# Kernel tuning notes

Measured on AMD Instinct MI355X. Metric: run time of the kernel, lower is better.

The kernel has to match this reference:

```python
import jax, jax.numpy as jnp
import numpy as np

B, H, W, DIM, NH = 4, 32, 32, 768, 12
HD = DIM // NH

def setup_inputs() -> dict:
    key = jax.random.key(0)
    ks = jax.random.split(key, 7)
    s = 0.02
    return {
        "x": jax.random.normal(ks[0], (B, H, W, DIM), dtype=jnp.float32),
        "qkv_w": jax.random.normal(ks[1], (3 * DIM, DIM), dtype=jnp.float32) * s,  # torch Linear (out,in)
        "qkv_b": jax.random.normal(ks[2], (3 * DIM,), dtype=jnp.float32) * s,
        "proj_w": jax.random.normal(ks[3], (DIM, DIM), dtype=jnp.float32) * s,
        "proj_b": jax.random.normal(ks[4], (DIM,), dtype=jnp.float32) * s,
        "rel_pos_h": jax.random.normal(ks[5], (2 * H - 1, HD), dtype=jnp.float32) * s,
        "rel_pos_w": jax.random.normal(ks[6], (2 * W - 1, HD), dtype=jnp.float32) * s,
    }

def _get_rel_pos(size, rel_pos):
    # q_size == k_size == size, rel_pos.shape[0] == 2*size-1 -> no interpolation
    idx = jnp.arange(size)[:, None] - jnp.arange(size)[None, :] + (size - 1)
    return rel_pos[idx]  # (size, size, head_dim)

def reference(x, qkv_w, qkv_b, proj_w, proj_b, rel_pos_h, rel_pos_w):
    b, h, w, c = x.shape
    hw = h * w
    hd = c // NH
    scale = hd ** -0.5  # SDPA default scale

    qkv = x @ qkv_w.T + qkv_b                       # (B,H,W,3C)
    qkv = qkv.reshape(b, hw, 3, NH, hd).transpose(2, 0, 3, 1, 4)  # (3,B,nh,HW,hd)
    q, k, v = qkv[0], qkv[1], qkv[2]                # each (B,nh,HW,hd)

    Rh = _get_rel_pos(h, rel_pos_h)                 # (H,H,hd)
    Rw = _get_rel_pos(w, rel_pos_w)                 # (W,W,hd)
    r_q = q.reshape(b, NH, h, w, hd)
    rel_h = jnp.einsum('bnhwc,hkc->bnhwk', r_q, Rh)  # (B,nh,H,W,H)
    rel_w = jnp.einsum('bnhwc,wkc->bnhwk', r_q, Rw)  # (B,nh,H,W,W)
    bias = (rel_h[..., :, None] + rel_w[..., None, :]).reshape(b, NH, hw, hw)

    attn = jnp.einsum('bnqd,bnkd->bnqk', q, k) * scale + bias
    attn = jax.nn.softmax(attn, axis=-1)
    out = jnp.einsum('bnqk,bnkd->bnqd', attn, v)    # (B,nh,HW,hd)
    out = out.reshape(b, NH, h, w, hd).transpose(0, 2, 3, 1, 4).reshape(b, h, w, c)
    return out @ proj_w.T + proj_b
```

## Files before the change

### kernel.cpp

```cpp
#include <hip/hip_runtime.h>
#include <stdint.h>

typedef unsigned short u16;
typedef __attribute__((ext_vector_type(8))) short short8;
typedef __attribute__((ext_vector_type(8))) u16 ushort8;
typedef __attribute__((ext_vector_type(4))) float f32x4;
typedef __attribute__((ext_vector_type(16))) float f32x16;
typedef __attribute__((ext_vector_type(4))) unsigned int uint4v;

#define LOG2E 1.44269504088896f

__device__ __forceinline__ u16 f2bf(float f) {
  unsigned int u = __builtin_bit_cast(unsigned int, f);
  u += 0x7FFF + ((u >> 16) & 1);
  return (u16)(u >> 16);
}
__device__ __forceinline__ unsigned int cvtpk(float a, float b) {
  unsigned int r;
  asm("v_cvt_pk_bf16_f32 %0, %1, %2" : "=v"(r) : "v"(a), "v"(b));
  return r;
}
__device__ __forceinline__ void plswap(unsigned int& a, unsigned int& b) {
  asm("v_permlane32_swap_b32 %0, %1" : "+v"(a), "+v"(b));
}
__device__ __forceinline__ void gload_lds16(const u16* g, u16* l) {
  __builtin_amdgcn_global_load_lds((const __attribute__((address_space(1))) void*)g,
                                   (__attribute__((address_space(3))) void*)l, 16, 0, 0);
}

__global__ __launch_bounds__(256) void cvt_all(
    const float* __restrict__ s0, u16* __restrict__ d0, int n0,
    const float* __restrict__ s1, u16* __restrict__ d1, int n1,
    const float* __restrict__ s2, u16* __restrict__ d2, int n2,
    const float* __restrict__ s3, u16* __restrict__ d3, int n3,
    const float* __restrict__ s4, u16* __restrict__ d4, int n4) {
  const int tid0 = blockIdx.x * 256 + threadIdx.x;
  const int stride = gridDim.x * 256 * 4;
#define CVT_SEG(S, D, N)                                       \
  for (int i = tid0 * 4; i < (N); i += stride) {               \
    float4 v = *(const float4*)((S) + i);                      \
    *(uint2*)((D) + i) = make_uint2(cvtpk(v.x, v.y), cvtpk(v.z, v.w)); \
  }
  CVT_SEG(s0, d0, n0)
  CVT_SEG(s1, d1, n1)
  CVT_SEG(s2, d2, n2)
  CVT_SEG(s3, d3, n3)
  CVT_SEG(s4, d4, n4)
#undef CVT_SEG
}

#define CTS 130
__global__ __launch_bounds__(256) void gemm128q(
    const u16* __restrict__ A, const u16* __restrict__ B,
    const float* __restrict__ bias,
    u16* __restrict__ qo, u16* __restrict__ ko, u16* __restrict__ vto,
    int M, int N, int K) {
  __shared__ u16 smem[4 * 128 * 64];
  const int tid = threadIdx.x;
  const int lane = tid & 63, wave = tid >> 6;
  const int wr = wave >> 1, wc = wave & 1;
  const int l15 = lane & 15, l4 = lane >> 4;
  const int fid = blockIdx.y * gridDim.x + blockIdx.x;
  const int cpx = (gridDim.x * gridDim.y) >> 3;
  const int swz = (fid & 7) * cpx + (fid >> 3);
  const int bxs = swz % gridDim.x, bys = swz / gridDim.x;
  const int bm = bys << 7, bn = bxs << 7;
  f32x4 acc[4][4] = {};
  const int nkt = K >> 6;

#define STAGE(buf, kt)                                                        \
  {                                                                           \
    u16* As_ = smem + (buf) * 16384;                                          \
    u16* Bs_ = As_ + 8192;                                                    \
    const int k0_ = (kt) << 6;                                                \
    _Pragma("unroll") for (int j = 0; j < 4; ++j) {                           \
      const int cbase = j * 256 + wave * 64;                                  \
      const int chunk = cbase + lane;                                         \
      const int row = chunk >> 3;                                             \
      const int co = (((chunk & 7) ^ (row & 7)) << 3);                        \
      gload_lds16(A + (size_t)(bm + row) * K + k0_ + co, As_ + cbase * 8);    \
      gload_lds16(B + (size_t)(bn + row) * K + k0_ + co, Bs_ + cbase * 8);    \
    }                                                                         \
  }

  STAGE(0, 0)
  __syncthreads();
  int cur = 0;
  for (int kt = 0; kt < nkt; ++kt) {
    if (kt + 1 < nkt) STAGE(cur ^ 1, kt + 1)
    const u16* As = smem + cur * 16384;
    const u16* Bs = As + 8192;
    short8 af[2][4], bf[2][4];
#pragma unroll
    for (int kc = 0; kc < 2; ++kc)
#pragma unroll
      for (int i = 0; i < 4; ++i) {
        const int rA = wr * 64 + i * 16 + l15;
        const int rB = wc * 64 + i * 16 + l15;
        af[kc][i] = *(const short8*)((const char*)As +
            (((rA * 64 + kc * 32 + l4 * 8) * 2) ^ ((rA & 7) << 4)));
        bf[kc][i] = *(const short8*)((const char*)Bs +
            (((rB * 64 + kc * 32 + l4 * 8) * 2) ^ ((rB & 7) << 4)));
      }
#pragma unroll
    for (int kc = 0; kc < 2; ++kc)
#pragma unroll
      for (int mi = 0; mi < 4; ++mi)
#pragma unroll
        for (int ni = 0; ni < 4; ++ni)
          acc[mi][ni] = __builtin_amdgcn_mfma_f32_16x16x32_bf16(
              af[kc][mi], bf[kc][ni], acc[mi][ni], 0, 0, 0);
    __syncthreads();
    cur ^= 1;
  }
#undef STAGE

  u16* ct = smem;
  const int which = bn / 768;
  const float sc = (which == 0) ? 0.125f * LOG2E : 1.0f;
#pragma unroll
  for (int ni = 0; ni < 4; ++ni) {
    const int col = wc * 64 + ni * 16 + l15;
    const float bv = bias[bn + col];
#pragma unroll
    for (int mi = 0; mi < 4; ++mi)
#pragma unroll
      for (int j = 0; j < 4; ++j) {
        const int row = wr * 64 + mi * 16 + l4 * 4 + j;
        ct[row * CTS + col] = f2bf((acc[mi][ni][j] + bv) * sc);
      }
  }
  __syncthreads();
  const int nrel = bn - which * 768;
  const int head0 = nrel >> 6;
  const int b = bm >> 10;
  if (which < 2) {
    u16* dst0 = which ? ko : qo;
    const int row = tid >> 1, hp = tid & 1;
    const int head = head0 + hp;
    const int pos = (bm + row) & 1023;
    const u16* s = ct + row * CTS + hp * 64;
    u16* base = dst0 + ((size_t)(b * 12 + head)) * 65536;
    if (which == 0) {
      const int qsub = pos >> 5, lq = pos & 31;
#pragma unroll
      for (int g = 0; g < 8; ++g) {
        const int c = g >> 1, hi = g & 1;
        *(ushort8*)(base + ((qsub * 4 + c) * 64 + hi * 32 + lq) * 8) =
            *(const ushort8*)(s + g * 8);
      }
    } else {
      const int t = pos >> 6, hf = (pos >> 5) & 1, lq = pos & 31;
#pragma unroll
      for (int g = 0; g < 8; ++g) {
        const int c = g >> 1, hi = g & 1;
        *(ushort8*)(base + (((t * 4 + c) * 2 + hf) * 64 + hi * 32 + lq) * 8) =
            *(const ushort8*)(s + g * 8);
      }
    }
  } else {
    const int c = tid >> 1, seg = tid & 1;
    const int head = head0 + (c >> 6), dd = c & 63;
    const int posbase = (bm & 1023) + seg * 64;
    const int t = posbase >> 6;
    const int half = dd >> 5, lqd = dd & 31;
    u16* base = vto + ((size_t)(b * 12 + head)) * 65536;
    const u16* s = ct + (seg * 64) * CTS + c;
#pragma unroll
    for (int g = 0; g < 8; ++g) {
      ushort8 o;
#pragma unroll
      for (int e = 0; e < 8; ++e) o[e] = s[(g * 8 + e) * CTS];
      *(ushort8*)(base + (((t * 4 + (g >> 1)) * 2 + half) * 64 + (g & 1) * 32 + lqd) * 8) = o;
    }
  }
}

__global__ __launch_bounds__(256) void gemm64(
    const u16* __restrict__ A, const u16* __restrict__ B,
    const float* __restrict__ bias, float* __restrict__ fout,
    int M, int N, int K) {
  __shared__ u16 smem[2 * 8192];
  const int tid = threadIdx.x;
  const int lane = tid & 63, wave = tid >> 6;
  const int wr = wave >> 1, wc = wave & 1;
  const int l15 = lane & 15, l4 = lane >> 4;
  const int fid = blockIdx.y * gridDim.x + blockIdx.x;
  const int cpx = (gridDim.x * gridDim.y) >> 3;
  const int swz = (fid & 7) * cpx + (fid >> 3);
  const int bxs = swz % gridDim.x, bys = swz / gridDim.x;
  const int bm = bys << 6, bn = bxs << 6;
  f32x4 acc[2][2] = {};
  const int nkt = K >> 6;

#define STAGE64(buf, kt)                                                      \
  {                                                                           \
    u16* As_ = smem + (buf) * 8192;                                           \
    u16* Bs_ = As_ + 4096;                                                    \
    const int k0_ = (kt) << 6;                                                \
    _Pragma("unroll") for (int j = 0; j < 2; ++j) {                           \
      const int cbase = j * 256 + wave * 64;                                  \
      const int chunk = cbase + lane;                                         \
      const int row = chunk >> 3;                                             \
      const int co = (((chunk & 7) ^ (row & 7)) << 3);                        \
      gload_lds16(A + (size_t)(bm + row) * K + k0_ + co, As_ + cbase * 8);    \
      gload_lds16(B + (size_t)(bn + row) * K + k0_ + co, Bs_ + cbase * 8);    \
    }                                                                         \
  }

  STAGE64(0, 0)
  __syncthreads();
  int cur = 0;
  for (int kt = 0; kt < nkt; ++kt) {
    if (kt + 1 < nkt) STAGE64(cur ^ 1, kt + 1)
    const u16* As = smem + cur * 8192;
    const u16* Bs = As + 4096;
    short8 af[2][2], bf[2][2];
#pragma unroll
    for (int kc = 0; kc < 2; ++kc)
#pragma unroll
      for (int i = 0; i < 2; ++i) {
        const int rA = wr * 32 + i * 16 + l15;
        const int rB = wc * 32 + i * 16 + l15;
        af[kc][i] = *(const short8*)((const char*)As +
            (((rA * 64 + kc * 32 + l4 * 8) * 2) ^ ((rA & 7) << 4)));
        bf[kc][i] = *(const short8*)((const char*)Bs +
            (((rB * 64 + kc * 32 + l4 * 8) * 2) ^ ((rB & 7) << 4)));
      }
#pragma unroll
    for (int kc = 0; kc < 2; ++kc)
#pragma unroll
      for (int mi = 0; mi < 2; ++mi)
#pragma unroll
        for (int ni = 0; ni < 2; ++ni)
          acc[mi][ni] = __builtin_amdgcn_mfma_f32_16x16x32_bf16(
              af[kc][mi], bf[kc][ni], acc[mi][ni], 0, 0, 0);
    __syncthreads();
    cur ^= 1;
  }
#undef STAGE64

#pragma unroll
  for (int ni = 0; ni < 2; ++ni) {
    const int col = wc * 32 + ni * 16 + l15;
    const float bv = bias[bn + col];
#pragma unroll
    for (int mi = 0; mi < 2; ++mi)
#pragma unroll
      for (int j = 0; j < 4; ++j) {
        const int row = wr * 32 + mi * 16 + l4 * 4 + j;
        fout[(size_t)(bm + row) * N + bn + col] = acc[mi][ni][j] + bv;
      }
  }
}

__global__ __launch_bounds__(64) void rel_kernel(
    const u16* __restrict__ pq, const u16* __restrict__ th,
    const u16* __restrict__ tw, float* __restrict__ rhp, float* __restrict__ rwp) {
  const int bh = blockIdx.x, h = blockIdx.y, type = blockIdx.z;
  const int lane = threadIdx.x & 63, lq = lane & 31, hi = lane >> 5;
  short8 qf[4];
#pragma unroll
  for (int c = 0; c < 4; ++c)
    qf[c] = *(const short8*)(pq + (size_t)bh * 65536 + ((h * 4 + c) * 64 + lane) * 8);
  if (type == 0) {
    const int tr = h - lq + 31;
    f32x16 acc{};
#pragma unroll
    for (int c = 0; c < 4; ++c) {
      short8 bfr = *(const short8*)(th + tr * 64 + c * 16 + hi * 8);
      acc = __builtin_amdgcn_mfma_f32_32x32x16_bf16(qf[c], bfr, acc, 0, 0, 0);
    }
    float* O = rhp + (size_t)bh * 32768 + lq * 1024 + h * 32;
#pragma unroll
    for (int r = 0; r < 16; ++r) {
      const int w = (r & 3) + 8 * (r >> 2) + 4 * hi;
      O[w] = acc[r] * 8.0f;
    }
  } else {
    const int r0 = lq;
    const int r1 = (lq == 31) ? 62 : (32 + lq);
    f32x16 a0{}, a1{};
#pragma unroll
    for (int c = 0; c < 4; ++c) {
      short8 b0 = *(const short8*)(tw + r0 * 64 + c * 16 + hi * 8);
      short8 b1 = *(const short8*)(tw + r1 * 64 + c * 16 + hi * 8);
      a0 = __builtin_amdgcn_mfma_f32_32x32x16_bf16(qf[c], b0, a0, 0, 0, 0);
      a1 = __builtin_amdgcn_mfma_f32_32x32x16_bf16(qf[c], b1, a1, 0, 0, 0);
    }
    float* O = rwp + (size_t)bh * 32768 + h * 32;
#pragma unroll
    for (int r = 0; r < 16; ++r) {
      const int w = (r & 3) + 8 * (r >> 2) + 4 * hi;
      const int k0i = w - lq + 31;
      const int k1i = w - lq - 1;
      if (k0i >= 0 && k0i < 32) O[k0i * 1024 + w] = a0[r] * 8.0f;
      if (k1i >= 0) O[k1i * 1024 + w] = a1[r] * 8.0f;
    }
  }
}

__global__ __launch_bounds__(256) void attn_kernel(
    const u16* __restrict__ pq, const u16* __restrict__ pk,
    const u16* __restrict__ pv, const float* __restrict__ rhp,
    const float* __restrict__ rwp, u16* __restrict__ aout) {
  const int bh = blockIdx.x, qt = blockIdx.y;
  const int tid = threadIdx.x, lane = tid & 63, wave = tid >> 6;
  const int wq = wave >> 1, wk = wave & 1;
  const int lq = lane & 31, hi = lane >> 5;
  const int q0 = qt * 64 + wq * 32;
  const u16* Qb = pq + (size_t)bh * 65536;
  const u16* Kb = pk + (size_t)bh * 65536;
  const u16* Vb = pv + (size_t)bh * 65536;
  const float* RH = rhp + (size_t)bh * 32768;
  const float* RW = rwp + (size_t)bh * 32768;
  __shared__ float part[2][2][64][17];
  __shared__ float lsums[2][2][32];
  const int qg = q0 + lq;
  const int qsub = qt * 2 + wq;
  short8 qf[4];
#pragma unroll
  for (int c = 0; c < 4; ++c)
    qf[c] = *(const short8*)(Qb + ((qsub * 4 + c) * 64 + lane) * 8);
  float rw[16];
#pragma unroll
  for (int r = 0; r < 16; ++r)
    rw[r] = RW[((r & 3) + 8 * (r >> 2) + 4 * hi) * 1024 + qg];
  f32x16 o0{}, o1{};
  float lsum = 0.f;
  short8 kf[2][8];
  {
    const int t0 = wk * 8;
#pragma unroll
    for (int c = 0; c < 4; ++c) {
      kf[0][c]     = *(const short8*)(Kb + (((t0 * 4 + c) * 2 + 0) * 64 + lane) * 8);
      kf[0][4 + c] = *(const short8*)(Kb + (((t0 * 4 + c) * 2 + 1) * 64 + lane) * 8);
    }
  }
#pragma unroll
  for (int t = 0; t < 8; ++t) {
    const int tt = wk * 8 + t;
    const int cur = t & 1, nxt = cur ^ 1;
    short8 vb0[4], vb1[4];
#pragma unroll
    for (int cc = 0; cc < 4; ++cc) {
      vb0[cc] = *(const short8*)(Vb + (((tt * 4 + cc) * 2 + 0) * 64 + lane) * 8);
      vb1[cc] = *(const short8*)(Vb + (((tt * 4 + cc) * 2 + 1) * 64 + lane) * 8);
    }
    const float rh0 = RH[(tt * 2) * 1024 + qg];
    const float rh1 = RH[(tt * 2 + 1) * 1024 + qg];
    if (t < 7) {
      const int tn = tt + 1;
#pragma unroll
      for (int c = 0; c < 4; ++c) {
        kf[nxt][c]     = *(const short8*)(Kb + (((tn * 4 + c) * 2 + 0) * 64 + lane) * 8);
        kf[nxt][4 + c] = *(const short8*)(Kb + (((tn * 4 + c) * 2 + 1) * 64 + lane) * 8);
      }
    }
    f32x16 s0{}, s1{};
    __builtin_amdgcn_s_setprio(1);
#pragma unroll
    for (int c = 0; c < 4; ++c) {
      s0 = __builtin_amdgcn_mfma_f32_32x32x16_bf16(kf[cur][c], qf[c], s0, 0, 0, 0);
      s1 = __builtin_amdgcn_mfma_f32_32x32x16_bf16(kf[cur][4 + c], qf[c], s1, 0, 0, 0);
    }
    __builtin_amdgcn_s_setprio(0);
    float b0[16], b1[16];
#pragma unroll
    for (int r = 0; r < 16; ++r) { b0[r] = rh0 + rw[r]; b1[r] = rh1 + rw[r]; }
#pragma unroll
    for (int r = 0; r < 16; ++r) {
      s0[r] = exp2f(s0[r] + b0[r]);
      s1[r] = exp2f(s1[r] + b1[r]);
    }
#pragma unroll
    for (int r = 0; r < 16; ++r) lsum += s0[r] + s1[r];
    unsigned int pw[16];
#pragma unroll
    for (int j = 0; j < 8; ++j) pw[j] = cvtpk(s0[2 * j], s0[2 * j + 1]);
#pragma unroll
    for (int j = 0; j < 8; ++j) pw[8 + j] = cvtpk(s1[2 * j], s1[2 * j + 1]);
    plswap(pw[0], pw[2]);  plswap(pw[1], pw[3]);
    plswap(pw[4], pw[6]);  plswap(pw[5], pw[7]);
    plswap(pw[8], pw[10]); plswap(pw[9], pw[11]);
    plswap(pw[12], pw[14]); plswap(pw[13], pw[15]);
    __builtin_amdgcn_s_setprio(1);
#pragma unroll
    for (int cc = 0; cc < 4; ++cc) {
      uint4v w4 = {pw[cc * 4 + 0], pw[cc * 4 + 1], pw[cc * 4 + 2], pw[cc * 4 + 3]};
      short8 pa = __builtin_bit_cast(short8, w4);
      o0 = __builtin_amdgcn_mfma_f32_32x32x16_bf16(pa, vb0[cc], o0, 0, 0, 0);
      o1 = __builtin_amdgcn_mfma_f32_32x32x16_bf16(pa, vb1[cc], o1, 0, 0, 0);
    }
    __builtin_amdgcn_s_setprio(0);
  }
  lsum += __shfl_xor(lsum, 32, 64);
  if (hi == 0) lsums[wq][wk][lq] = lsum;
#pragma unroll
  for (int r = 0; r < 16; ++r)
    part[wq][wk][lane][r] = wk ? o0[r] : o1[r];
  __syncthreads();
  const int b = bh / 12, head = bh - b * 12;
  u16* outp = aout + (size_t)b * 1024 * 768 + head * 64 + wk * 32;
#pragma unroll
  for (int r = 0; r < 16; ++r) {
    const int qr = (r & 3) + 8 * (r >> 2) + 4 * hi;
    const float inv = 1.0f / (lsums[wq][0][qr] + lsums[wq][1][qr]);
    const float own = wk ? o1[r] : o0[r];
    const float val = own + part[wq][wk ^ 1][lane][r];
    outp[(size_t)(q0 + qr) * 768 + lq] = f2bf(val * inv);
  }
}

extern "C" void kernel_launch(void* const* d_in, const int* in_sizes, int n_in,
                              void* d_out, int out_size, void* d_ws, size_t ws_size,
                              hipStream_t stream) {
  const float* x = (const float*)d_in[0];
  const float* qkv_w = (const float*)d_in[1];
  const float* qkv_b = (const float*)d_in[2];
  const float* proj_w = (const float*)d_in[3];
  const float* proj_b = (const float*)d_in[4];
  const float* rph = (const float*)d_in[5];
  const float* rpw = (const float*)d_in[6];
  float* out = (float*)d_out;
  char* ws = (char*)d_ws;
  u16* xb     = (u16*)(ws + 0);
  u16* wqkv   = (u16*)(ws + 6291456);
  u16* wproj  = (u16*)(ws + 9830400);
  u16* pq     = (u16*)(ws + 11010048);
  u16* pk     = (u16*)(ws + 17301504);
  u16* pv     = (u16*)(ws + 23592960);
  float* rhp  = (float*)(ws + 29884416);
  float* rwp  = (float*)(ws + 36175872);
  u16* aout   = (u16*)(ws + 42467328);
  u16* rphb   = (u16*)(ws + 48758784);
  u16* rpwb   = (u16*)(ws + 48766848);

  cvt_all<<<1024, 256, 0, stream>>>(x, xb, 3145728, qkv_w, wqkv, 1769472,
                                    proj_w, wproj, 589824, rph, rphb, 4032,
                                    rpw, rpwb, 4032);
  gemm128q<<<dim3(18, 32), 256, 0, stream>>>(xb, wqkv, qkv_b, pq, pk, pv,
                                             4096, 2304, 768);
  rel_kernel<<<dim3(48, 32, 2), 64, 0, stream>>>(pq, rphb, rpwb, rhp, rwp);
  attn_kernel<<<dim3(48, 16), 256, 0, stream>>>(pq, pk, pv, rhp, rwp, aout);
  gemm64<<<dim3(12, 64), 256, 0, stream>>>(aout, wproj, proj_b, out,
                                           4096, 768, 768);
}
```

Before: 87.68 us.

## Fuse rel_w bias computation into attention kernel via LDS

The rel_w bias is no longer produced by rel_kernel and read back from global memory. Instead, the wk==0 waves of each attention block compute Q·Rw^T with MFMA, stage the result in shared memory, and gather the diagonal-shifted values per lane after a barrier. rel_kernel now launches only the rel_h half, and the rh values are preloaded into registers before the loop. This removes a global write/read round trip and half of rel_kernel's work. In exchange it adds LDS use, a __syncthreads, and a serial prologue on half the waves of attn_kernel.

```diff
diff --git a/kernel.cpp b/kernel.cpp
--- a/kernel.cpp
+++ b/kernel.cpp
@@ -256,54 +256,32 @@
 
 __global__ __launch_bounds__(64) void rel_kernel(
     const u16* __restrict__ pq, const u16* __restrict__ th,
-    const u16* __restrict__ tw, float* __restrict__ rhp, float* __restrict__ rwp) {
-  const int bh = blockIdx.x, h = blockIdx.y, type = blockIdx.z;
+    float* __restrict__ rhp) {
+  const int bh = blockIdx.x, h = blockIdx.y;
   const int lane = threadIdx.x & 63, lq = lane & 31, hi = lane >> 5;
   short8 qf[4];
 #pragma unroll
   for (int c = 0; c < 4; ++c)
     qf[c] = *(const short8*)(pq + (size_t)bh * 65536 + ((h * 4 + c) * 64 + lane) * 8);
-  if (type == 0) {
-    const int tr = h - lq + 31;
-    f32x16 acc{};
-#pragma unroll
-    for (int c = 0; c < 4; ++c) {
-      short8 bfr = *(const short8*)(th + tr * 64 + c * 16 + hi * 8);
-      acc = __builtin_amdgcn_mfma_f32_32x32x16_bf16(qf[c], bfr, acc, 0, 0, 0);
-    }
-    float* O = rhp + (size_t)bh * 32768 + lq * 1024 + h * 32;
-#pragma unroll
-    for (int r = 0; r < 16; ++r) {
-      const int w = (r & 3) + 8 * (r >> 2) + 4 * hi;
-      O[w] = acc[r] * 8.0f;
-    }
-  } else {
-    const int r0 = lq;
-    const int r1 = (lq == 31) ? 62 : (32 + lq);
-    f32x16 a0{}, a1{};
-#pragma unroll
-    for (int c = 0; c < 4; ++c) {
-      short8 b0 = *(const short8*)(tw + r0 * 64 + c * 16 + hi * 8);
-      short8 b1 = *(const short8*)(tw + r1 * 64 + c * 16 + hi * 8);
-      a0 = __builtin_amdgcn_mfma_f32_32x32x16_bf16(qf[c], b0, a0, 0, 0, 0);
-      a1 = __builtin_amdgcn_mfma_f32_32x32x16_bf16(qf[c], b1, a1, 0, 0, 0);
-    }
-    float* O = rwp + (size_t)bh * 32768 + h * 32;
-#pragma unroll
-    for (int r = 0; r < 16; ++r) {
-      const int w = (r & 3) + 8 * (r >> 2) + 4 * hi;
-      const int k0i = w - lq + 31;
-      const int k1i = w - lq - 1;
-      if (k0i >= 0 && k0i < 32) O[k0i * 1024 + w] = a0[r] * 8.0f;
-      if (k1i >= 0) O[k1i * 1024 + w] = a1[r] * 8.0f;
-    }
+  const int tr = h - lq + 31;
+  f32x16 acc{};
+#pragma unroll
+  for (int c = 0; c < 4; ++c) {
+    short8 bfr = *(const short8*)(th + tr * 64 + c * 16 + hi * 8);
+    acc = __builtin_amdgcn_mfma_f32_32x32x16_bf16(qf[c], bfr, acc, 0, 0, 0);
+  }
+  float* O = rhp + (size_t)bh * 32768 + lq * 1024 + h * 32;
+#pragma unroll
+  for (int r = 0; r < 16; ++r) {
+    const int w = (r & 3) + 8 * (r >> 2) + 4 * hi;
+    O[w] = acc[r] * 8.0f;
   }
 }
 
 __global__ __launch_bounds__(256) void attn_kernel(
     const u16* __restrict__ pq, const u16* __restrict__ pk,
     const u16* __restrict__ pv, const float* __restrict__ rhp,
-    const float* __restrict__ rwp, u16* __restrict__ aout) {
+    const u16* __restrict__ tw, u16* __restrict__ aout) {
   const int bh = blockIdx.x, qt = blockIdx.y;
   const int tid = threadIdx.x, lane = tid & 63, wave = tid >> 6;
   const int wq = wave >> 1, wk = wave & 1;
@@ -313,21 +291,15 @@
   const u16* Kb = pk + (size_t)bh * 65536;
   const u16* Vb = pv + (size_t)bh * 65536;
   const float* RH = rhp + (size_t)bh * 32768;
-  const float* RW = rwp + (size_t)bh * 32768;
   __shared__ float part[2][2][64][17];
   __shared__ float lsums[2][2][32];
+  __shared__ float pd_lds[2][64][32];
   const int qg = q0 + lq;
   const int qsub = qt * 2 + wq;
   short8 qf[4];
 #pragma unroll
   for (int c = 0; c < 4; ++c)
     qf[c] = *(const short8*)(Qb + ((qsub * 4 + c) * 64 + lane) * 8);
-  float rw[16];
-#pragma unroll
-  for (int r = 0; r < 16; ++r)
-    rw[r] = RW[((r & 3) + 8 * (r >> 2) + 4 * hi) * 1024 + qg];
-  f32x16 o0{}, o1{};
-  float lsum = 0.f;
   short8 kf[2][8];
   {
     const int t0 = wk * 8;
@@ -337,6 +309,34 @@
       kf[0][4 + c] = *(const short8*)(Kb + (((t0 * 4 + c) * 2 + 1) * 64 + lane) * 8);
     }
   }
+  if (wk == 0) {
+    f32x16 pa{}, pb{};
+    const int trB = (lq == 31) ? 62 : 32 + lq;
+#pragma unroll
+    for (int c = 0; c < 4; ++c) {
+      short8 ta = *(const short8*)(tw + (lq * 64 + c * 16 + hi * 8));
+      short8 tb = *(const short8*)(tw + (trB * 64 + c * 16 + hi * 8));
+      pa = __builtin_amdgcn_mfma_f32_32x32x16_bf16(ta, qf[c], pa, 0, 0, 0);
+      pb = __builtin_amdgcn_mfma_f32_32x32x16_bf16(tb, qf[c], pb, 0, 0, 0);
+    }
+#pragma unroll
+    for (int r = 0; r < 16; ++r) {
+      const int j = (r & 3) + 8 * (r >> 2) + 4 * hi;
+      pd_lds[wq][j][lq] = pa[r] * 8.0f;
+      pd_lds[wq][32 + j][lq] = pb[r] * 8.0f;
+    }
+  }
+  float rhv[16];
+#pragma unroll
+  for (int i = 0; i < 16; ++i)
+    rhv[i] = RH[(16 * wk + i) * 1024 + qg];
+  __syncthreads();
+  float rw[16];
+#pragma unroll
+  for (int r = 0; r < 16; ++r)
+    rw[r] = pd_lds[wq][lq + 31 - ((r & 3) + 8 * (r >> 2) + 4 * hi)][lq];
+  f32x16 o0{}, o1{};
+  float lsum = 0.f;
 #pragma unroll
   for (int t = 0; t < 8; ++t) {
     const int tt = wk * 8 + t;
@@ -347,8 +347,6 @@
       vb0[cc] = *(const short8*)(Vb + (((tt * 4 + cc) * 2 + 0) * 64 + lane) * 8);
       vb1[cc] = *(const short8*)(Vb + (((tt * 4 + cc) * 2 + 1) * 64 + lane) * 8);
     }
-    const float rh0 = RH[(tt * 2) * 1024 + qg];
-    const float rh1 = RH[(tt * 2 + 1) * 1024 + qg];
     if (t < 7) {
       const int tn = tt + 1;
 #pragma unroll
@@ -365,13 +363,11 @@
       s1 = __builtin_amdgcn_mfma_f32_32x32x16_bf16(kf[cur][4 + c], qf[c], s1, 0, 0, 0);
     }
     __builtin_amdgcn_s_setprio(0);
-    float b0[16], b1[16];
-#pragma unroll
-    for (int r = 0; r < 16; ++r) { b0[r] = rh0 + rw[r]; b1[r] = rh1 + rw[r]; }
+    const float rh0 = rhv[2 * t], rh1 = rhv[2 * t + 1];
 #pragma unroll
     for (int r = 0; r < 16; ++r) {
-      s0[r] = exp2f(s0[r] + b0[r]);
-      s1[r] = exp2f(s1[r] + b1[r]);
+      s0[r] = exp2f(s0[r] + (rh0 + rw[r]));
+      s1[r] = exp2f(s1[r] + (rh1 + rw[r]));
     }
 #pragma unroll
     for (int r = 0; r < 16; ++r) lsum += s0[r] + s1[r];
@@ -431,7 +427,6 @@
   u16* pk     = (u16*)(ws + 17301504);
   u16* pv     = (u16*)(ws + 23592960);
   float* rhp  = (float*)(ws + 29884416);
-  float* rwp  = (float*)(ws + 36175872);
   u16* aout   = (u16*)(ws + 42467328);
   u16* rphb   = (u16*)(ws + 48758784);
   u16* rpwb   = (u16*)(ws + 48766848);
@@ -441,8 +436,8 @@
                                     rpw, rpwb, 4032);
   gemm128q<<<dim3(18, 32), 256, 0, stream>>>(xb, wqkv, qkv_b, pq, pk, pv,
                                              4096, 2304, 768);
-  rel_kernel<<<dim3(48, 32, 2), 64, 0, stream>>>(pq, rphb, rpwb, rhp, rwp);
-  attn_kernel<<<dim3(48, 16), 256, 0, stream>>>(pq, pk, pv, rhp, rwp, aout);
+  rel_kernel<<<dim3(48, 32), 64, 0, stream>>>(pq, rphb, rhp);
+  attn_kernel<<<dim3(48, 16), 256, 0, stream>>>(pq, pk, pv, rhp, rpwb, aout);
   gemm64<<<dim3(12, 64), 256, 0, stream>>>(aout, wproj, proj_b, out,
                                            4096, 768, 768);
 }
```

Measured after the change: 81.61 us. 6.9% less time.
